# Optimization experiments

Measured on AMD Instinct MI355X. Metric: run time of the kernel, lower is better.

Reference implementation:

```python
import jax, jax.numpy as jnp
import numpy as np

B, S, D_MODEL, D_K = 4, 4096, 1024, 64


def setup_inputs() -> dict:
    key = jax.random.key(0)
    kx, kq, kk, kv = jax.random.split(key, 4)
    x = jax.random.normal(kx, (B, S, D_MODEL), dtype=jnp.float32)
    # Linear(in, out) stores weight as (out, in); y = x @ W^T, no bias
    Wq = jax.random.normal(kq, (D_K, D_MODEL), dtype=jnp.float32) * (D_MODEL ** -0.5)
    Wk = jax.random.normal(kk, (D_K, D_MODEL), dtype=jnp.float32) * (D_MODEL ** -0.5)
    Wv = jax.random.normal(kv, (D_MODEL, D_MODEL), dtype=jnp.float32) * (D_MODEL ** -0.5)
    return {"x": x, "Wq": Wq, "Wk": Wk, "Wv": Wv}


def reference(x, Wq, Wk, Wv):
    # single-head scaled dot-product attention
    q = jnp.einsum('bsd,kd->bsk', x, Wq)   # [B,S,d_k]
    k = jnp.einsum('bsd,kd->bsk', x, Wk)   # [B,S,d_k]
    v = jnp.einsum('bsd,md->bsm', x, Wv)   # [B,S,d_model]
    scale = 1.0 / jnp.sqrt(jnp.asarray(q.shape[-1], q.dtype))
    scores = jnp.einsum('bqk,bsk->bqs', q, k) * scale  # [B,S,S]
    probs = jax.nn.softmax(scores, axis=-1)
    return jnp.einsum('bqs,bsm->bqm', probs, v)        # [B,S,d_model]
```

## Files before the change

### kernel.cpp

```cpp
#include <hip/hip_runtime.h>


#define DEV static __device__ __forceinline__

typedef __attribute__((ext_vector_type(8))) short bf16x8;
typedef __attribute__((ext_vector_type(4))) float f32x4;
typedef __attribute__((ext_vector_type(4))) unsigned short u16x4;
typedef __attribute__((ext_vector_type(8))) unsigned short u16x8;
typedef __attribute__((address_space(1))) void as1_void;
typedef __attribute__((address_space(3))) void as3_void;

DEV unsigned short f2bf(float f) {
  union { float f; unsigned u; } v; v.f = f;
  return (unsigned short)((v.u + 0x7FFFu + ((v.u >> 16) & 1u)) >> 16);
}

DEV unsigned pk_bf16(float a, float b) {
  union { float f; unsigned u; } va, vb;
  va.f = a; vb.f = b;
  return __builtin_amdgcn_perm(vb.u + 0x8000u, va.u + 0x8000u, 0x07060302u);
}

DEV void gload16(const void* g, void* l) {
  __builtin_amdgcn_global_load_lds((as1_void*)g, (as3_void*)l, 16, 0, 0);
}

DEV int swz(int row, int cb) { return (row << 7) + (cb ^ ((row & 7) << 4)); }

__global__ __launch_bounds__(256) void cast_all_k(
    const float* __restrict__ x, const float* __restrict__ wq,
    const float* __restrict__ wk, const float* __restrict__ wv,
    unsigned short* __restrict__ xb, unsigned short* __restrict__ wcat, float sq) {
  const int stride = gridDim.x * blockDim.x;
  for (int i = blockIdx.x * blockDim.x + threadIdx.x; i < 2244608; i += stride) {
    const float* src; unsigned short* dst; float scale; int j;
    if (i < 2097152)      { src = x;  dst = xb;            scale = 1.f; j = i; }
    else if (i < 2105344) { src = wq; dst = wcat;          scale = sq;  j = i - 2097152; }
    else if (i < 2113536) { src = wk; dst = wcat + 65536;  scale = 1.f; j = i - 2105344; }
    else                  { src = wv; dst = wcat + 131072; scale = 1.f; j = i - 2113536; }
    const float4* p = (const float4*)src + (size_t)j * 2;
    float4 a = p[0], b = p[1];
    u16x8 r;
    r[0] = f2bf(a.x * scale); r[1] = f2bf(a.y * scale);
    r[2] = f2bf(a.z * scale); r[3] = f2bf(a.w * scale);
    r[4] = f2bf(b.x * scale); r[5] = f2bf(b.y * scale);
    r[6] = f2bf(b.z * scale); r[7] = f2bf(b.w * scale);
    *(u16x8*)(dst + (size_t)j * 8) = r;
  }
}

__global__ __launch_bounds__(256, 2) void gemm_qkv_k(
    const unsigned short* __restrict__ xb, const unsigned short* __restrict__ wcat,
    unsigned short* __restrict__ qk, unsigned short* __restrict__ vT) {
  __shared__ __align__(16) unsigned char smem[65536];
  unsigned char* sA = smem;
  unsigned char* sB = smem + 32768;
  const int tid = threadIdx.x;
  const int w = tid >> 6, lane = tid & 63, lo = lane & 15, hi = lane >> 4;
  const int wr = w >> 1, wc = w & 1;
  const int bn = blockIdx.x, m0 = blockIdx.y * 128, n0 = bn * 128;
  const char* aBase = (const char*)xb + (size_t)m0 * 2048;
  const char* bBase = (const char*)wcat + (size_t)n0 * 2048;

  const int soff = ((w * 4) << 10) + (lane << 4);
  f32x4 acc[4][4];
  const f32x4 z = {0.f, 0.f, 0.f, 0.f};
#pragma unroll
  for (int mi = 0; mi < 4; ++mi)
#pragma unroll
    for (int ni = 0; ni < 4; ++ni) acc[mi][ni] = z;

#pragma unroll
  for (int r2 = 0; r2 < 4; ++r2) {
    const int off = soff + (r2 << 10);
    const int row = off >> 7;
    const int cbs = (off & 127) ^ ((row & 7) << 4);
    gload16(aBase + (size_t)row * 2048 + cbs, sA + ((w * 4 + r2) << 10));
    gload16(bBase + (size_t)row * 2048 + cbs, sB + ((w * 4 + r2) << 10));
  }
  __syncthreads();

  int cur = 0;
  for (int k0 = 0; k0 < 1024; k0 += 64) {
    if (k0 + 64 < 1024) {
      const int nb = (cur ^ 1) * 16384;
#pragma unroll
      for (int r2 = 0; r2 < 4; ++r2) {
        const int off = soff + (r2 << 10);
        const int row = off >> 7;
        const int cbs = (off & 127) ^ ((row & 7) << 4);
        gload16(aBase + (size_t)row * 2048 + (k0 + 64) * 2 + cbs, sA + nb + ((w * 4 + r2) << 10));
        gload16(bBase + (size_t)row * 2048 + (k0 + 64) * 2 + cbs, sB + nb + ((w * 4 + r2) << 10));
      }
    }
    const int cb0 = cur * 16384;
#pragma unroll
    for (int kk = 0; kk < 2; ++kk) {
      const int cb = kk * 64 + hi * 16;
      bf16x8 af[4], bfv[4];
#pragma unroll
      for (int mi = 0; mi < 4; ++mi)
        af[mi] = *(const bf16x8*)(sA + cb0 + swz(wr * 64 + mi * 16 + lo, cb));
#pragma unroll
      for (int ni = 0; ni < 4; ++ni)
        bfv[ni] = *(const bf16x8*)(sB + cb0 + swz(wc * 64 + ni * 16 + lo, cb));
#pragma unroll
      for (int mi = 0; mi < 4; ++mi)
#pragma unroll
        for (int ni = 0; ni < 4; ++ni)
          acc[mi][ni] = __builtin_amdgcn_mfma_f32_16x16x32_bf16(af[mi], bfv[ni], acc[mi][ni], 0, 0, 0);
    }
    __syncthreads();
    cur ^= 1;
  }

  if (bn == 0) {
#pragma unroll
    for (int mi = 0; mi < 4; ++mi) {
      const int row = m0 + wr * 64 + mi * 16 + hi * 4;
#pragma unroll
      for (int ni = 0; ni < 4; ++ni) {
        const int col = wc * 64 + ni * 16 + lo;
#pragma unroll
        for (int r = 0; r < 4; ++r)
          qk[(size_t)(row + r) * 128 + col] = f2bf(acc[mi][ni][r]);
      }
    }
  } else {
#pragma unroll
    for (int mi = 0; mi < 4; ++mi) {
      const int grow = m0 + wr * 64 + mi * 16 + hi * 4;
      const int b = grow >> 12, s = grow & 4095;
#pragma unroll
      for (int ni = 0; ni < 4; ++ni) {
        const int vcol = (n0 - 128) + wc * 64 + ni * 16 + lo;
        u16x4 pk;
#pragma unroll
        for (int r = 0; r < 4; ++r) pk[r] = f2bf(acc[mi][ni][r]);
        *(u16x4*)(vT + (size_t)(b * 1024 + vcol) * 4096 + s) = pk;
      }
    }
  }
}

__global__ __launch_bounds__(512, 4) void pv_k(
    const unsigned short* __restrict__ qk, const unsigned short* __restrict__ vT,
    float* __restrict__ out) {
  __shared__ __align__(16) unsigned char smem[65536];
  unsigned char* sK = smem;
  unsigned char* sV = smem + 16384;
  unsigned char* sP = smem + 49152;
  const int tid = threadIdx.x;
  const int w = tid >> 6, lane = tid & 63, lo = lane & 15, hi = lane >> 4;
  const int wr = w >> 2, wc = w & 3;
  const int ck = blockIdx.x, qt = blockIdx.y, b = blockIdx.z;
  const char* qkB = (const char*)qk;
  const char* vTB = (const char*)vT;
  const size_t qrow0 = (size_t)(b * 4096 + qt * 128);
  const f32x4 z = {0.f, 0.f, 0.f, 0.f};

  const int q = w * 16 + lo;
  bf16x8 qf[2];
#pragma unroll
  for (int kk = 0; kk < 2; ++kk)
    qf[kk] = *(const bf16x8*)(qkB + (qrow0 + q) * 256 + kk * 64 + hi * 16);
  float lsum = 0.f;

  const int kc = w * 64 + lane;
  const int kRow = kc >> 3, kG = kc & 7;
  const char* kSrc = qkB + (size_t)(b * 4096 + kRow) * 256 + 128 + ((kG ^ (kRow & 7)) << 4);
  unsigned char* kDst = sK + (kc << 4);

  const char* vSrcJ[4];
#pragma unroll
  for (int j = 0; j < 4; ++j) {
    const int c = tid + j * 512;
    const int row = c >> 3, g = c & 7;
    vSrcJ[j] = vTB + (size_t)(b * 1024 + ck * 256 + row) * 8192 + ((g ^ (row & 7)) << 4);
  }

  const int qx7 = (q & 7) << 4;
  const int aP0 = (q << 7) + (((0 + (hi >> 1)) << 4) ^ qx7) + ((hi & 1) << 3);
  const int aP1 = (q << 7) + (((2 + (hi >> 1)) << 4) ^ qx7) + ((hi & 1) << 3);
  const int aP2 = (q << 7) + (((4 + (hi >> 1)) << 4) ^ qx7) + ((hi & 1) << 3);
  const int aP3 = (q << 7) + (((6 + (hi >> 1)) << 4) ^ qx7) + ((hi & 1) << 3);

  f32x4 acc[4][4];
#pragma unroll
  for (int mi = 0; mi < 4; ++mi)
#pragma unroll
    for (int ni = 0; ni < 4; ++ni) acc[mi][ni] = z;

#pragma unroll
  for (int j = 0; j < 4; ++j) gload16(vSrcJ[j], sV + ((tid + j * 512) << 4));
  gload16(kSrc, kDst);
  __syncthreads();

  int cur = 0;
  for (int t = 0; t < 64; ++t) {
    gload16(kSrc + (size_t)((t + 1) & 63) * 16384, kDst + (cur ^ 1) * 8192);
    f32x4 sv[4];
    sv[0] = z; sv[1] = z; sv[2] = z; sv[3] = z;
#pragma unroll
    for (int kk = 0; kk < 2; ++kk) {
#pragma unroll
      for (int n = 0; n < 4; ++n) {
        bf16x8 kf = *(const bf16x8*)(sK + cur * 8192 + swz(n * 16 + lo, kk * 64 + hi * 16));
        sv[n] = __builtin_amdgcn_mfma_f32_16x16x32_bf16(kf, qf[kk], sv[n], 0, 0, 0);
      }
    }
    {
      const float p0 = __builtin_amdgcn_exp2f(sv[0][0]);
      const float p1 = __builtin_amdgcn_exp2f(sv[0][1]);
      const float p2 = __builtin_amdgcn_exp2f(sv[0][2]);
      const float p3 = __builtin_amdgcn_exp2f(sv[0][3]);
      const float p4 = __builtin_amdgcn_exp2f(sv[1][0]);
      const float p5 = __builtin_amdgcn_exp2f(sv[1][1]);
      const float p6 = __builtin_amdgcn_exp2f(sv[1][2]);
      const float p7 = __builtin_amdgcn_exp2f(sv[1][3]);
      const float p8 = __builtin_amdgcn_exp2f(sv[2][0]);
      const float p9 = __builtin_amdgcn_exp2f(sv[2][1]);
      const float pa_ = __builtin_amdgcn_exp2f(sv[2][2]);
      const float pb_ = __builtin_amdgcn_exp2f(sv[2][3]);
      const float pc_ = __builtin_amdgcn_exp2f(sv[3][0]);
      const float pd_ = __builtin_amdgcn_exp2f(sv[3][1]);
      const float pe_ = __builtin_amdgcn_exp2f(sv[3][2]);
      const float pf_ = __builtin_amdgcn_exp2f(sv[3][3]);
      lsum += (((p0 + p1) + (p2 + p3)) + ((p4 + p5) + (p6 + p7))) +
              (((p8 + p9) + (pa_ + pb_)) + ((pc_ + pd_) + (pe_ + pf_)));
      uint2 d0, d1, d2, d3;
      d0.x = pk_bf16(p0, p1);  d0.y = pk_bf16(p2, p3);
      d1.x = pk_bf16(p4, p5);  d1.y = pk_bf16(p6, p7);
      d2.x = pk_bf16(p8, p9);  d2.y = pk_bf16(pa_, pb_);
      d3.x = pk_bf16(pc_, pd_); d3.y = pk_bf16(pe_, pf_);
      *(uint2*)(sP + aP0) = d0;
      *(uint2*)(sP + aP1) = d1;
      *(uint2*)(sP + aP2) = d2;
      *(uint2*)(sP + aP3) = d3;
    }
    asm volatile("s_waitcnt vmcnt(1) lgkmcnt(0)" ::: "memory");
    __builtin_amdgcn_sched_barrier(0);
    __builtin_amdgcn_s_barrier();
    __builtin_amdgcn_sched_barrier(0);
    __builtin_amdgcn_s_setprio(1);
#pragma unroll
    for (int kk = 0; kk < 2; ++kk) {
      bf16x8 pa[4];
#pragma unroll
      for (int mi = 0; mi < 4; ++mi)
        pa[mi] = *(const bf16x8*)(sP + swz(wr * 64 + mi * 16 + lo, kk * 64 + hi * 16));
#pragma unroll
      for (int ni = 0; ni < 4; ++ni) {
        bf16x8 vf = *(const bf16x8*)(sV + swz(wc * 64 + ni * 16 + lo, kk * 64 + hi * 16));
#pragma unroll
        for (int mi = 0; mi < 4; ++mi)
          acc[mi][ni] = __builtin_amdgcn_mfma_f32_16x16x32_bf16(pa[mi], vf, acc[mi][ni], 0, 0, 0);
      }
    }
    __builtin_amdgcn_s_setprio(0);
    __syncthreads();
    if (t < 63) {
#pragma unroll
      for (int j = 0; j < 4; ++j)
        gload16(vSrcJ[j] + (size_t)(t + 1) * 128, sV + ((tid + j * 512) << 4));
    }
    cur ^= 1;
  }

  lsum += __shfl_xor(lsum, 16, 64);
  lsum += __shfl_xor(lsum, 32, 64);
  float* lLds = (float*)smem;
  if (hi == 0) lLds[q] = lsum;
  __syncthreads();

#pragma unroll
  for (int mi = 0; mi < 4; ++mi)
#pragma unroll
    for (int r = 0; r < 4; ++r) {
      const int rloc = wr * 64 + mi * 16 + hi * 4 + r;
      const int grow = (int)qrow0 + rloc;
      const float linv = 1.0f / lLds[rloc];
#pragma unroll
      for (int ni = 0; ni < 4; ++ni) {
        const int col = ck * 256 + wc * 64 + ni * 16 + lo;
        out[(size_t)grow * 1024 + col] = acc[mi][ni][r] * linv;
      }
    }
}

extern "C" void kernel_launch(void* const* d_in, const int* in_sizes, int n_in,
                              void* d_out, int out_size, void* d_ws, size_t ws_size,
                              hipStream_t stream) {
  const float* x  = (const float*)d_in[0];
  const float* Wq = (const float*)d_in[1];
  const float* Wk = (const float*)d_in[2];
  const float* Wv = (const float*)d_in[3];

  char* ws = (char*)d_ws;
  unsigned short* xb    = (unsigned short*)(ws);
  unsigned short* wcat  = (unsigned short*)(ws + 33554432);
  unsigned short* qk    = (unsigned short*)(ws + 35913728);
  unsigned short* vT    = (unsigned short*)(ws + 40108032);

  const float SCALE_Q = 0.125f * 1.4426950408889634f;

  cast_all_k<<<2048, 256, 0, stream>>>(x, Wq, Wk, Wv, xb, wcat, SCALE_Q);
  gemm_qkv_k<<<dim3(9, 128), 256, 0, stream>>>(xb, wcat, qk, vT);
  pv_k<<<dim3(4, 32, 4), 512, 0, stream>>>(qk, vT, (float*)d_out);
}
```

Measured before the change: 240.2 us.

## Software-pipeline QK/exp of next tile with PV MFMAs using double-buffered P

Double-buffers the P tile in shared memory and computes QK scores and exp for tile t+1 in the same phase as the PV MFMAs for tile t. The K prefetch distance grows to two tiles. The aim is to overlap the exp/VALU work with the matrix work and remove one barrier-separated phase per iteration. In exchange, LDS per block grows to 80 KB, which reduces the number of blocks that can be resident per CU, and register pressure rises.

```diff
diff --git a/kernel.cpp b/kernel.cpp
--- a/kernel.cpp
+++ b/kernel.cpp
@@ -146,7 +146,7 @@
 __global__ __launch_bounds__(512, 4) void pv_k(
     const unsigned short* __restrict__ qk, const unsigned short* __restrict__ vT,
     float* __restrict__ out) {
-  __shared__ __align__(16) unsigned char smem[65536];
+  __shared__ __align__(16) unsigned char smem[81920];
   unsigned char* sK = smem;
   unsigned char* sV = smem + 16384;
   unsigned char* sP = smem + 49152;
@@ -191,64 +191,74 @@
 #pragma unroll
     for (int ni = 0; ni < 4; ++ni) acc[mi][ni] = z;
 
+#define QK_EXP(KBUF, PB)                                                               \
+  {                                                                                    \
+    f32x4 sv[4];                                                                       \
+    sv[0] = z; sv[1] = z; sv[2] = z; sv[3] = z;                                        \
+    _Pragma("unroll")                                                                  \
+    for (int kk = 0; kk < 2; ++kk) {                                                   \
+      _Pragma("unroll")                                                                \
+      for (int n = 0; n < 4; ++n) {                                                    \
+        bf16x8 kf = *(const bf16x8*)(sK + (KBUF) * 8192 + swz(n * 16 + lo, kk * 64 + hi * 16)); \
+        sv[n] = __builtin_amdgcn_mfma_f32_16x16x32_bf16(kf, qf[kk], sv[n], 0, 0, 0);   \
+      }                                                                                \
+    }                                                                                  \
+    const float p0 = __builtin_amdgcn_exp2f(sv[0][0]);                                 \
+    const float p1 = __builtin_amdgcn_exp2f(sv[0][1]);                                 \
+    const float p2 = __builtin_amdgcn_exp2f(sv[0][2]);                                 \
+    const float p3 = __builtin_amdgcn_exp2f(sv[0][3]);                                 \
+    const float p4 = __builtin_amdgcn_exp2f(sv[1][0]);                                 \
+    const float p5 = __builtin_amdgcn_exp2f(sv[1][1]);                                 \
+    const float p6 = __builtin_amdgcn_exp2f(sv[1][2]);                                 \
+    const float p7 = __builtin_amdgcn_exp2f(sv[1][3]);                                 \
+    const float p8 = __builtin_amdgcn_exp2f(sv[2][0]);                                 \
+    const float p9 = __builtin_amdgcn_exp2f(sv[2][1]);                                 \
+    const float pa_ = __builtin_amdgcn_exp2f(sv[2][2]);                                \
+    const float pb_ = __builtin_amdgcn_exp2f(sv[2][3]);                                \
+    const float pc_ = __builtin_amdgcn_exp2f(sv[3][0]);                                \
+    const float pd_ = __builtin_amdgcn_exp2f(sv[3][1]);                                \
+    const float pe_ = __builtin_amdgcn_exp2f(sv[3][2]);                                \
+    const float pf_ = __builtin_amdgcn_exp2f(sv[3][3]);                                \
+    lsum += (((p0 + p1) + (p2 + p3)) + ((p4 + p5) + (p6 + p7))) +                      \
+            (((p8 + p9) + (pa_ + pb_)) + ((pc_ + pd_) + (pe_ + pf_)));                 \
+    uint2 d0, d1, d2, d3;                                                              \
+    d0.x = pk_bf16(p0, p1);   d0.y = pk_bf16(p2, p3);                                  \
+    d1.x = pk_bf16(p4, p5);   d1.y = pk_bf16(p6, p7);                                  \
+    d2.x = pk_bf16(p8, p9);   d2.y = pk_bf16(pa_, pb_);                                \
+    d3.x = pk_bf16(pc_, pd_); d3.y = pk_bf16(pe_, pf_);                                \
+    unsigned char* pbase = sP + (PB) * 16384;                                          \
+    *(uint2*)(pbase + aP0) = d0;                                                       \
+    *(uint2*)(pbase + aP1) = d1;                                                       \
+    *(uint2*)(pbase + aP2) = d2;                                                       \
+    *(uint2*)(pbase + aP3) = d3;                                                       \
+  }
+
 #pragma unroll
   for (int j = 0; j < 4; ++j) gload16(vSrcJ[j], sV + ((tid + j * 512) << 4));
   gload16(kSrc, kDst);
+  gload16(kSrc + 16384, kDst + 8192);
   __syncthreads();
+  QK_EXP(0, 0)
+  asm volatile("s_waitcnt lgkmcnt(0)" ::: "memory");
+  __builtin_amdgcn_sched_barrier(0);
+  __builtin_amdgcn_s_barrier();
+  __builtin_amdgcn_sched_barrier(0);
 
   int cur = 0;
   for (int t = 0; t < 64; ++t) {
-    gload16(kSrc + (size_t)((t + 1) & 63) * 16384, kDst + (cur ^ 1) * 8192);
-    f32x4 sv[4];
-    sv[0] = z; sv[1] = z; sv[2] = z; sv[3] = z;
-#pragma unroll
-    for (int kk = 0; kk < 2; ++kk) {
-#pragma unroll
-      for (int n = 0; n < 4; ++n) {
-        bf16x8 kf = *(const bf16x8*)(sK + cur * 8192 + swz(n * 16 + lo, kk * 64 + hi * 16));
-        sv[n] = __builtin_amdgcn_mfma_f32_16x16x32_bf16(kf, qf[kk], sv[n], 0, 0, 0);
-      }
-    }
-    {
-      const float p0 = __builtin_amdgcn_exp2f(sv[0][0]);
-      const float p1 = __builtin_amdgcn_exp2f(sv[0][1]);
-      const float p2 = __builtin_amdgcn_exp2f(sv[0][2]);
-      const float p3 = __builtin_amdgcn_exp2f(sv[0][3]);
-      const float p4 = __builtin_amdgcn_exp2f(sv[1][0]);
-      const float p5 = __builtin_amdgcn_exp2f(sv[1][1]);
-      const float p6 = __builtin_amdgcn_exp2f(sv[1][2]);
-      const float p7 = __builtin_amdgcn_exp2f(sv[1][3]);
-      const float p8 = __builtin_amdgcn_exp2f(sv[2][0]);
-      const float p9 = __builtin_amdgcn_exp2f(sv[2][1]);
-      const float pa_ = __builtin_amdgcn_exp2f(sv[2][2]);
-      const float pb_ = __builtin_amdgcn_exp2f(sv[2][3]);
-      const float pc_ = __builtin_amdgcn_exp2f(sv[3][0]);
-      const float pd_ = __builtin_amdgcn_exp2f(sv[3][1]);
-      const float pe_ = __builtin_amdgcn_exp2f(sv[3][2]);
-      const float pf_ = __builtin_amdgcn_exp2f(sv[3][3]);
-      lsum += (((p0 + p1) + (p2 + p3)) + ((p4 + p5) + (p6 + p7))) +
-              (((p8 + p9) + (pa_ + pb_)) + ((pc_ + pd_) + (pe_ + pf_)));
-      uint2 d0, d1, d2, d3;
-      d0.x = pk_bf16(p0, p1);  d0.y = pk_bf16(p2, p3);
-      d1.x = pk_bf16(p4, p5);  d1.y = pk_bf16(p6, p7);
-      d2.x = pk_bf16(p8, p9);  d2.y = pk_bf16(pa_, pb_);
-      d3.x = pk_bf16(pc_, pd_); d3.y = pk_bf16(pe_, pf_);
-      *(uint2*)(sP + aP0) = d0;
-      *(uint2*)(sP + aP1) = d1;
-      *(uint2*)(sP + aP2) = d2;
-      *(uint2*)(sP + aP3) = d3;
-    }
+    gload16(kSrc + (size_t)((t + 2) & 63) * 16384, kDst + cur * 8192);
     asm volatile("s_waitcnt vmcnt(1) lgkmcnt(0)" ::: "memory");
     __builtin_amdgcn_sched_barrier(0);
     __builtin_amdgcn_s_barrier();
     __builtin_amdgcn_sched_barrier(0);
     __builtin_amdgcn_s_setprio(1);
+    if (t < 63) QK_EXP(cur ^ 1, cur ^ 1)
 #pragma unroll
     for (int kk = 0; kk < 2; ++kk) {
       bf16x8 pa[4];
 #pragma unroll
       for (int mi = 0; mi < 4; ++mi)
-        pa[mi] = *(const bf16x8*)(sP + swz(wr * 64 + mi * 16 + lo, kk * 64 + hi * 16));
+        pa[mi] = *(const bf16x8*)(sP + cur * 16384 + swz(wr * 64 + mi * 16 + lo, kk * 64 + hi * 16));
 #pragma unroll
       for (int ni = 0; ni < 4; ++ni) {
         bf16x8 vf = *(const bf16x8*)(sV + swz(wc * 64 + ni * 16 + lo, kk * 64 + hi * 16));
@@ -258,7 +268,10 @@
       }
     }
     __builtin_amdgcn_s_setprio(0);
-    __syncthreads();
+    asm volatile("s_waitcnt lgkmcnt(0)" ::: "memory");
+    __builtin_amdgcn_sched_barrier(0);
+    __builtin_amdgcn_s_barrier();
+    __builtin_amdgcn_sched_barrier(0);
     if (t < 63) {
 #pragma unroll
       for (int j = 0; j < 4; ++j)
@@ -266,9 +279,11 @@
     }
     cur ^= 1;
   }
+#undef QK_EXP
 
   lsum += __shfl_xor(lsum, 16, 64);
   lsum += __shfl_xor(lsum, 32, 64);
+  __syncthreads();
   float* lLds = (float*)smem;
   if (hi == 0) lLds[q] = lsum;
   __syncthreads();
```

Measured after the change: 244.8 us. Within noise of the previous version (+1.9%).
